# Kernel optimization log

Hardware: AMD Instinct MI355X
Metric: run time of the kernel (lower is better)

## Reference

```python
import jax, jax.numpy as jnp
import numpy as np


def _conv(x, w):
    # x: [B,H,W,Cin], w: [kh,kw,Cin,Cout] -> [B,H,W,Cout], stride 1, SAME
    return jax.lax.conv_general_dilated(
        x, w, window_strides=(1, 1), padding='SAME',
        dimension_numbers=('NHWC', 'HWIO', 'NHWC'))


def _convlstm_step(x, h, c, wx, wh, bias):
    # gates in Keras ConvLSTM2D order: i, f, c(g), o
    gates = _conv(x, wx) + _conv(h, wh) + bias
    i_g, f_g, g_g, o_g = jnp.split(gates, 4, axis=-1)
    i_g = jax.nn.sigmoid(i_g)
    f_g = jax.nn.sigmoid(f_g)
    g_g = jnp.tanh(g_g)
    o_g = jax.nn.sigmoid(o_g)
    c_new = f_g * c + i_g * g_g
    h_new = o_g * jnp.tanh(c_new)
    return h_new, c_new


def setup_inputs() -> dict:
    key = jax.random.key(0)
    ks = jax.random.split(key, 6)
    B, H, W = 64, 32, 32
    CIN, HID, K, L = 64, 128, 3, 3
    x = jax.random.normal(ks[0], (B, H, W, CIN), dtype=jnp.float32)
    hs = jax.random.normal(ks[1], (L, B, H, W, HID), dtype=jnp.float32)
    cs = jax.random.normal(ks[2], (L, B, H, W, HID), dtype=jnp.float32)
    Wx = jax.random.normal(ks[3], (L, K, K, CIN, 4 * HID), dtype=jnp.float32) * 0.05
    Wh = jax.random.normal(ks[4], (L, K, K, HID, 4 * HID), dtype=jnp.float32) * 0.05
    b = jnp.zeros((L, 4 * HID), dtype=jnp.float32)
    return {'x': x, 'hs': hs, 'cs': cs, 'Wx': Wx, 'Wh': Wh, 'b': b,
            'num_repeats': 3}


def reference(x, hs, cs, Wx, Wh, b, num_repeats):
    L = Wx.shape[0]
    hs_l = [hs[i] for i in range(L)]
    cs_l = [cs[i] for i in range(L)]
    for _ in range(num_repeats):
        for i in range(L):
            # NOTE: every layer consumes the raw input x (faithful to source)
            hs_l[i], cs_l[i] = _convlstm_step(x, hs_l[i], cs_l[i],
                                              Wx[i], Wh[i], b[i])
    hs_out = jnp.stack(hs_l, axis=0)
    cs_out = jnp.stack(cs_l, axis=0)
    return (hs_l[-1], hs_out, cs_out)
```

## Files before the change

### kernel.cpp

```cpp
#include <hip/hip_runtime.h>
#include <cstddef>

typedef __bf16 bf16_t;
typedef __bf16 bf16x8 __attribute__((ext_vector_type(8)));
typedef float  f32x4  __attribute__((ext_vector_type(4)));

#define NB     64
#define IMG_H  32
#define IMG_W  32
#define PH     34
#define PW     34
#define CX     64
#define CHID   128
#define NPIX   (NB*IMG_H*IMG_W)
#define PADPIX (NB*PH*PW)
#define KT_TOT 54

#define XPAD_ELEMS   ((size_t)PADPIX*CX)
#define HPAD_ELEMS   ((size_t)PADPIX*CHID)
#define WCAT_L_ELEMS ((size_t)KT_TOT*512*32)
#define XPAD_BYTES   (XPAD_ELEMS*2)
#define HPAD_BYTES   (HPAD_ELEMS*2)

#define HW_STATE     ((size_t)NPIX*CHID)

#define OFF_XPAD 0
#define OFF_HPAD (OFF_XPAD + XPAD_BYTES)
#define OFF_WCAT (OFF_HPAD + 6*HPAD_BYTES)
#define OFF_BPERM (OFF_WCAT + 3*WCAT_L_ELEMS*2)
#define WS_NEEDED (OFF_BPERM + 3*512*4)

__device__ __forceinline__ void async16(const void* g, void* l) {
  __builtin_amdgcn_global_load_lds(
      (const __attribute__((address_space(1))) void*)g,
      (__attribute__((address_space(3))) void*)l, 16, 0, 0);
}

__device__ __forceinline__ float fsig(float x) {
  return __builtin_amdgcn_rcpf(1.f + __expf(-x));
}
__device__ __forceinline__ float ftanh(float x) {
  return 1.f - 2.f * __builtin_amdgcn_rcpf(1.f + __expf(2.f * x));
}

__global__ __launch_bounds__(256) void pad_x_kernel(const float* __restrict__ x,
                                                    bf16_t* __restrict__ xp) {
  int idx = blockIdx.x * 256 + threadIdx.x;
  if (idx >= PADPIX * (CX / 8)) return;
  int g = idx & 7;
  int r = idx >> 3;
  int px = r % PW; r /= PW;
  int py = r % PH;
  int b  = r / PH;
  int iy = py - 1, ix = px - 1;
  bf16x8 v;
  if ((unsigned)iy < 32u && (unsigned)ix < 32u) {
    const float* s = x + ((((size_t)b * 32 + iy) * 32 + ix) * CX + g * 8);
#pragma unroll
    for (int j = 0; j < 8; ++j) v[j] = (bf16_t)s[j];
  } else {
#pragma unroll
    for (int j = 0; j < 8; ++j) v[j] = (bf16_t)0.f;
  }
  *(bf16x8*)(xp + (size_t)idx * 8) = v;
}

__global__ __launch_bounds__(256) void pad_h_kernel(const float* __restrict__ hs,
                                                    bf16_t* __restrict__ hp) {
  const int PER_L = PADPIX * (CHID / 8);
  int idx = blockIdx.x * 256 + threadIdx.x;
  if (idx >= 3 * PER_L) return;
  int l   = idx / PER_L;
  int rix = idx - l * PER_L;
  int g = rix & 15;
  int r = rix >> 4;
  int px = r % PW; r /= PW;
  int py = r % PH;
  int b  = r / PH;
  int iy = py - 1, ix = px - 1;
  bf16x8 v;
  if ((unsigned)iy < 32u && (unsigned)ix < 32u) {
    const float* s = hs + ((((size_t)l * NB + b) * 32 + iy) * 32 + ix) * CHID + g * 8;
#pragma unroll
    for (int j = 0; j < 8; ++j) v[j] = (bf16_t)s[j];
  } else {
#pragma unroll
    for (int j = 0; j < 8; ++j) v[j] = (bf16_t)0.f;
  }
  bf16_t* base = hp + (size_t)l * 2 * HPAD_ELEMS + (size_t)rix * 8;
  *(bf16x8*)base = v;
  *(bf16x8*)(base + HPAD_ELEMS) = v;
}

__global__ __launch_bounds__(256) void wcat_kernel(const float* __restrict__ Wx,
                                                   const float* __restrict__ Wh,
                                                   const float* __restrict__ bias,
                                                   bf16_t* __restrict__ wt,
                                                   float* __restrict__ bp) {
  int idx = blockIdx.x * 256 + threadIdx.x;
  if (idx < 3 * 512) {
    int i = idx >> 9, np = idx & 511;
    int j0 = np >> 7, g = (np >> 5) & 3, rr = np & 31;
    int n = g * 128 + j0 * 32 + rr;
    bp[idx] = bias[i * 512 + n];
  }
  if (idx >= 3 * KT_TOT * 512 * 4) return;
  int kb = idx & 3;
  int r  = idx >> 2;
  int np = r & 511; r >>= 9;
  int kt = r % KT_TOT;
  int i  = r / KT_TOT;
  int j0 = np >> 7, g = (np >> 5) & 3, rr = np & 31;
  int n = g * 128 + j0 * 32 + rr;
  const float* src;
  int dy, dx, cin0, cdim;
  if (kt < 18) {
    dy = kt / 6; int rem = kt % 6; dx = rem >> 1; cin0 = (rem & 1) << 5;
    cdim = CX;  src = Wx + (size_t)i * 9 * CX * 512;
  } else {
    int t = kt - 18;
    dy = t / 12; int rem = t % 12; dx = rem >> 2; cin0 = (rem & 3) << 5;
    cdim = CHID; src = Wh + (size_t)i * 9 * CHID * 512;
  }
  src += ((size_t)(dy * 3 + dx) * cdim + cin0 + kb * 8) * 512 + n;
  bf16x8 v;
#pragma unroll
  for (int j = 0; j < 8; ++j) v[j] = (bf16_t)src[(size_t)j * 512];
  *(bf16x8*)(wt + (size_t)idx * 8) = v;
}

__global__ __launch_bounds__(256) void step_kernel(
    const bf16_t* __restrict__ xp,
    bf16_t* __restrict__ hpBase,
    const bf16_t* __restrict__ wtBase,
    const float* __restrict__ bpBase,
    float* __restrict__ csOut,
    float* __restrict__ hsOut,
    int parity) {
  __shared__ __align__(16) char lds[16384];
  char* ldsA = lds;
  char* ldsB = lds + 8192;

  const int tid  = threadIdx.x;
  const int w    = tid >> 6;
  const int lane = tid & 63;
  const int ln   = lane & 15;
  const int quad = lane >> 4;

  const int bid   = blockIdx.x;
  const int l     = bid >> 11;
  const int inner = bid & 2047;
  const int nblk  = inner & 3;
  const int tm    = inner >> 2;
  const int b     = tm >> 3;
  const int y0    = (tm & 7) << 2;

  const bf16_t* hin  = hpBase + (size_t)(l * 2 + parity) * HPAD_ELEMS;
  bf16_t*       hout = hpBase + (size_t)(l * 2 + (parity ^ 1)) * HPAD_ELEMS;
  const bf16_t* wt   = wtBase + (size_t)l * WCAT_L_ELEMS;
  const float*  bpl  = bpBase + l * 512;
  float*        cst  = csOut + (size_t)l * HW_STATE;
  float*        hst  = hsOut + (size_t)l * HW_STATE;

  const int cSw = (((lane & 3) ^ ((lane >> 3) & 3)) * 8);
  const int p0  = w * 16 + (lane >> 2);
  const int ppx = p0 & 31;
  const int ppy = y0 + (p0 >> 5);

  const bf16_t* aX0 = xp  + ((size_t)(b * PH + ppy) * PW + ppx) * CX + cSw;
  const bf16_t* aX1 = xp  + ((size_t)(b * PH + ppy + 2) * PW + ppx) * CX + cSw;
  const bf16_t* aH0 = hin + ((size_t)(b * PH + ppy) * PW + ppx) * CHID + cSw;
  const bf16_t* aH1 = hin + ((size_t)(b * PH + ppy + 2) * PW + ppx) * CHID + cSw;
  const bf16_t* bsrcBase = wt + (size_t)nblk * 4096 + w * 512 + (lane >> 2) * 32 + cSw;

  char* dstA0 = ldsA + w * 1024;
  char* dstA1 = ldsA + 4096 + w * 1024;
  char* dstB0 = ldsB + w * 1024;
  char* dstB1 = ldsB + 4096 + w * 1024;

  const int chunkRd = (quad ^ ((ln >> 1) & 3)) * 16;

  f32x4 acc[2][8];
#pragma unroll
  for (int s = 0; s < 8; ++s) {
    float bv = bpl[nblk * 128 + s * 16 + ln];
    f32x4 t = {bv, bv, bv, bv};
    acc[0][s] = t;
    acc[1][s] = t;
  }

  auto ktile = [&](const bf16_t* a0, const bf16_t* a1, const bf16_t* bs) {
    __syncthreads();
    async16(a0, dstA0);
    async16(a1, dstA1);
    async16(bs, dstB0);
    async16(bs + 2048, dstB1);
    __syncthreads();
    bf16x8 bv[8];
#pragma unroll
    for (int s = 0; s < 8; ++s)
      bv[s] = *(const bf16x8*)(ldsB + (s * 16 + ln) * 64 + chunkRd);
#pragma unroll
    for (int r = 0; r < 2; ++r) {
      bf16x8 av = *(const bf16x8*)(ldsA + (w * 32 + r * 16 + ln) * 64 + chunkRd);
#pragma unroll
      for (int s = 0; s < 8; ++s)
        acc[r][s] = __builtin_amdgcn_mfma_f32_16x16x32_bf16(av, bv[s], acc[r][s], 0, 0, 0);
    }
  };

  for (int dy = 0; dy < 3; ++dy)
    for (int dx = 0; dx < 3; ++dx) {
#pragma unroll
      for (int ck = 0; ck < 2; ++ck) {
        const int kt = (dy * 3 + dx) * 2 + ck;
        const int delta = (dy * PW + dx) * CX + ck * 32;
        ktile(aX0 + delta, aX1 + delta, bsrcBase + (size_t)kt * 16384);
      }
    }
  for (int dy = 0; dy < 3; ++dy)
    for (int dx = 0; dx < 3; ++dx) {
#pragma unroll
      for (int ck = 0; ck < 4; ++ck) {
        const int kt = 18 + (dy * 3 + dx) * 4 + ck;
        const int delta = (dy * PW + dx) * CHID + ck * 32;
        ktile(aH0 + delta, aH1 + delta, bsrcBase + (size_t)kt * 16384);
      }
    }

#pragma unroll
  for (int r = 0; r < 2; ++r) {
#pragma unroll
    for (int hh = 0; hh < 2; ++hh) {
      const int ch = nblk * 32 + hh * 16 + ln;
#pragma unroll
      for (int reg = 0; reg < 4; ++reg) {
        const int m = tm * 128 + w * 32 + r * 16 + quad * 4 + reg;
        float gi = acc[r][0 + hh][reg];
        float gf = acc[r][2 + hh][reg];
        float gg = acc[r][4 + hh][reg];
        float go = acc[r][6 + hh][reg];
        float ig = fsig(gi);
        float fg = fsig(gf);
        float gv = ftanh(gg);
        float og = fsig(go);
        size_t off = (size_t)m * CHID + ch;
        float cold = cst[off];
        float cnew = fg * cold + ig * gv;
        float hnew = og * ftanh(cnew);
        cst[off] = cnew;
        hst[off] = hnew;
        int yy = (m >> 5) & 31, xx = m & 31, bb = m >> 10;
        hout[((size_t)(bb * PH + yy + 1) * PW + xx + 1) * CHID + ch] = (bf16_t)hnew;
      }
    }
  }
}

extern "C" void kernel_launch(void* const* d_in, const int* in_sizes, int n_in,
                              void* d_out, int out_size, void* d_ws, size_t ws_size,
                              hipStream_t stream) {
  const float* x    = (const float*)d_in[0];
  const float* hs   = (const float*)d_in[1];
  const float* cs   = (const float*)d_in[2];
  const float* Wx   = (const float*)d_in[3];
  const float* Wh   = (const float*)d_in[4];
  const float* bias = (const float*)d_in[5];

  if (ws_size < (size_t)WS_NEEDED) return;

  char* ws = (char*)d_ws;
  bf16_t* xp = (bf16_t*)(ws + OFF_XPAD);
  bf16_t* hp = (bf16_t*)(ws + OFF_HPAD);
  bf16_t* wt = (bf16_t*)(ws + OFF_WCAT);
  float*  bp = (float*)(ws + OFF_BPERM);

  float* out    = (float*)d_out;
  float* h_last = out;
  float* hs_out = out + HW_STATE;
  float* cs_out = out + HW_STATE * 4;

  hipMemcpyAsync(cs_out, cs, 3 * HW_STATE * sizeof(float),
                 hipMemcpyDeviceToDevice, stream);
  pad_x_kernel<<<dim3((PADPIX * (CX / 8)) / 256), dim3(256), 0, stream>>>(x, xp);
  pad_h_kernel<<<dim3((3 * PADPIX * (CHID / 8)) / 256), dim3(256), 0, stream>>>(hs, hp);
  wcat_kernel<<<dim3((3 * KT_TOT * 512 * 4) / 256), dim3(256), 0, stream>>>(Wx, Wh, bias, wt, bp);

  for (int r = 0; r < 3; ++r) {
    step_kernel<<<dim3(3 * 2048), dim3(256), 0, stream>>>(
        xp, hp, wt, bp, cs_out, hs_out, r & 1);
  }

  hipMemcpyAsync(h_last, hs_out + 2 * HW_STATE, HW_STATE * sizeof(float),
                 hipMemcpyDeviceToDevice, stream);
}
```

Baseline: 1.720 ms.

## Double-buffer LDS k-tiles and double the M tile per block

Replaces the load-sync-compute-sync loop with a two-stage LDS ping-pong: the next k-tile is staged asynchronously while the current one feeds MFMAs, so only one barrier remains per iteration. Each block now covers 256 output pixels (8 image rows) instead of 128, which doubles weight reuse per B-tile load and halves the grid. The cost is more accumulator registers (4x8 f32x4) and 48KB of LDS per block, which the launch bound caps at two blocks per CU and may reduce occupancy.

After: 1.584 ms. -7.9%, faster.

```diff
diff --git a/kernel.cpp b/kernel.cpp
--- a/kernel.cpp
+++ b/kernel.cpp
@@ -129,7 +129,7 @@
   *(bf16x8*)(wt + (size_t)idx * 8) = v;
 }
 
-__global__ __launch_bounds__(256) void step_kernel(
+__global__ __launch_bounds__(256, 2) void step_kernel(
     const bf16_t* __restrict__ xp,
     bf16_t* __restrict__ hpBase,
     const bf16_t* __restrict__ wtBase,
@@ -137,9 +137,7 @@
     float* __restrict__ csOut,
     float* __restrict__ hsOut,
     int parity) {
-  __shared__ __align__(16) char lds[16384];
-  char* ldsA = lds;
-  char* ldsB = lds + 8192;
+  __shared__ __align__(16) char lds[2 * 24576];
 
   const int tid  = threadIdx.x;
   const int w    = tid >> 6;
@@ -148,12 +146,12 @@
   const int quad = lane >> 4;
 
   const int bid   = blockIdx.x;
-  const int l     = bid >> 11;
-  const int inner = bid & 2047;
+  const int l     = bid >> 10;
+  const int inner = bid & 1023;
   const int nblk  = inner & 3;
   const int tm    = inner >> 2;
-  const int b     = tm >> 3;
-  const int y0    = (tm & 7) << 2;
+  const int b     = tm >> 2;
+  const int y0    = (tm & 3) << 3;
 
   const bf16_t* hin  = hpBase + (size_t)(l * 2 + parity) * HPAD_ELEMS;
   bf16_t*       hout = hpBase + (size_t)(l * 2 + (parity ^ 1)) * HPAD_ELEMS;
@@ -168,74 +166,78 @@
   const int ppy = y0 + (p0 >> 5);
 
   const bf16_t* aX0 = xp  + ((size_t)(b * PH + ppy) * PW + ppx) * CX + cSw;
-  const bf16_t* aX1 = xp  + ((size_t)(b * PH + ppy + 2) * PW + ppx) * CX + cSw;
   const bf16_t* aH0 = hin + ((size_t)(b * PH + ppy) * PW + ppx) * CHID + cSw;
-  const bf16_t* aH1 = hin + ((size_t)(b * PH + ppy + 2) * PW + ppx) * CHID + cSw;
   const bf16_t* bsrcBase = wt + (size_t)nblk * 4096 + w * 512 + (lane >> 2) * 32 + cSw;
 
-  char* dstA0 = ldsA + w * 1024;
-  char* dstA1 = ldsA + 4096 + w * 1024;
-  char* dstB0 = ldsB + w * 1024;
-  char* dstB1 = ldsB + 4096 + w * 1024;
-
   const int chunkRd = (quad ^ ((ln >> 1) & 3)) * 16;
 
-  f32x4 acc[2][8];
+  f32x4 acc[4][8];
 #pragma unroll
   for (int s = 0; s < 8; ++s) {
     float bv = bpl[nblk * 128 + s * 16 + ln];
     f32x4 t = {bv, bv, bv, bv};
-    acc[0][s] = t;
-    acc[1][s] = t;
-  }
-
-  auto ktile = [&](const bf16_t* a0, const bf16_t* a1, const bf16_t* bs) {
-    __syncthreads();
-    async16(a0, dstA0);
-    async16(a1, dstA1);
-    async16(bs, dstB0);
-    async16(bs + 2048, dstB1);
-    __syncthreads();
+#pragma unroll
+    for (int r = 0; r < 4; ++r) acc[r][s] = t;
+  }
+
+  auto stage = [&](int kt, char* buf) {
+    char* Ab = buf;
+    char* Bb = buf + 16384;
+    if (kt < 18) {
+      const int tap = kt >> 1;
+      const int dy = tap / 3, dx = tap - dy * 3;
+      const bf16_t* s = aX0 + (dy * PW + dx) * CX + (kt & 1) * 32;
+#pragma unroll
+      for (int j = 0; j < 4; ++j)
+        async16(s + j * (2 * PW * CX), Ab + j * 4096 + w * 1024);
+    } else {
+      const int t = kt - 18;
+      const int tap = t >> 2;
+      const int dy = tap / 3, dx = tap - dy * 3;
+      const bf16_t* s = aH0 + (dy * PW + dx) * CHID + (t & 3) * 32;
+#pragma unroll
+      for (int j = 0; j < 4; ++j)
+        async16(s + j * (2 * PW * CHID), Ab + j * 4096 + w * 1024);
+    }
+    const bf16_t* bs = bsrcBase + (size_t)kt * 16384;
+    async16(bs, Bb + w * 1024);
+    async16(bs + 2048, Bb + 4096 + w * 1024);
+  };
+
+  auto compute = [&](const char* buf) {
+    const char* Ab = buf;
+    const char* Bb = buf + 16384;
     bf16x8 bv[8];
 #pragma unroll
     for (int s = 0; s < 8; ++s)
-      bv[s] = *(const bf16x8*)(ldsB + (s * 16 + ln) * 64 + chunkRd);
-#pragma unroll
-    for (int r = 0; r < 2; ++r) {
-      bf16x8 av = *(const bf16x8*)(ldsA + (w * 32 + r * 16 + ln) * 64 + chunkRd);
+      bv[s] = *(const bf16x8*)(Bb + (s * 16 + ln) * 64 + chunkRd);
+#pragma unroll
+    for (int r = 0; r < 4; ++r) {
+      bf16x8 av = *(const bf16x8*)(Ab + (w * 64 + r * 16 + ln) * 64 + chunkRd);
 #pragma unroll
       for (int s = 0; s < 8; ++s)
         acc[r][s] = __builtin_amdgcn_mfma_f32_16x16x32_bf16(av, bv[s], acc[r][s], 0, 0, 0);
     }
   };
 
-  for (int dy = 0; dy < 3; ++dy)
-    for (int dx = 0; dx < 3; ++dx) {
-#pragma unroll
-      for (int ck = 0; ck < 2; ++ck) {
-        const int kt = (dy * 3 + dx) * 2 + ck;
-        const int delta = (dy * PW + dx) * CX + ck * 32;
-        ktile(aX0 + delta, aX1 + delta, bsrcBase + (size_t)kt * 16384);
-      }
-    }
-  for (int dy = 0; dy < 3; ++dy)
-    for (int dx = 0; dx < 3; ++dx) {
-#pragma unroll
-      for (int ck = 0; ck < 4; ++ck) {
-        const int kt = 18 + (dy * 3 + dx) * 4 + ck;
-        const int delta = (dy * PW + dx) * CHID + ck * 32;
-        ktile(aH0 + delta, aH1 + delta, bsrcBase + (size_t)kt * 16384);
-      }
-    }
-
-#pragma unroll
-  for (int r = 0; r < 2; ++r) {
+  stage(0, lds);
+  __syncthreads();
+#pragma unroll 2
+  for (int kt = 0; kt < KT_TOT - 1; ++kt) {
+    stage(kt + 1, lds + ((kt + 1) & 1) * 24576);
+    compute(lds + (kt & 1) * 24576);
+    __syncthreads();
+  }
+  compute(lds + ((KT_TOT - 1) & 1) * 24576);
+
+#pragma unroll
+  for (int r = 0; r < 4; ++r) {
 #pragma unroll
     for (int hh = 0; hh < 2; ++hh) {
       const int ch = nblk * 32 + hh * 16 + ln;
 #pragma unroll
       for (int reg = 0; reg < 4; ++reg) {
-        const int m = tm * 128 + w * 32 + r * 16 + quad * 4 + reg;
+        const int m = tm * 256 + w * 64 + r * 16 + quad * 4 + reg;
         float gi = acc[r][0 + hh][reg];
         float gf = acc[r][2 + hh][reg];
         float gg = acc[r][4 + hh][reg];
@@ -287,7 +289,7 @@
   wcat_kernel<<<dim3((3 * KT_TOT * 512 * 4) / 256), dim3(256), 0, stream>>>(Wx, Wh, bias, wt, bp);
 
   for (int r = 0; r < 3; ++r) {
-    step_kernel<<<dim3(3 * 2048), dim3(256), 0, stream>>>(
+    step_kernel<<<dim3(3 * 1024), dim3(256), 0, stream>>>(
         xp, hp, wt, bp, cs_out, hs_out, r & 1);
   }
 
```
